# Kernel tuning notes

Hardware: AMD Instinct MI355X
Metric: run time of the kernel (lower is better)

The kernel has to match this reference:

```python
import jax, jax.numpy as jnp
import numpy as np

D_MODEL = 1024
NUM_HEADS = 16
MAX_SEQ_LEN = 2048
THETA = 10000.0
HEAD_DIM = D_MODEL // NUM_HEADS  # 64


def _trunc_normal(key, shape, std):
    # truncated normal in [-3, 3] sigma, matching nn.init.trunc_normal_
    return std * jax.random.truncated_normal(key, -3.0, 3.0, shape, dtype=jnp.float32)


def setup_inputs() -> dict:
    key = jax.random.key(0)
    kx, kq, kk, kv, ko = jax.random.split(key, 5)
    B, L = 2, 2048
    sigma = np.sqrt(2.0 / (D_MODEL + D_MODEL))
    x = jax.random.normal(kx, (B, L, D_MODEL), dtype=jnp.float32)
    token_positions = jnp.arange(L, dtype=jnp.int64 if jax.config.jax_enable_x64 else jnp.int32)[None, :]
    return {
        "x": x,
        "wq": _trunc_normal(kq, (D_MODEL, D_MODEL), sigma),
        "wk": _trunc_normal(kk, (D_MODEL, D_MODEL), sigma),
        "wv": _trunc_normal(kv, (D_MODEL, D_MODEL), sigma),
        "wo": _trunc_normal(ko, (D_MODEL, D_MODEL), sigma),
        "token_positions": token_positions,
    }


def _rope_tables():
    pos = jnp.arange(MAX_SEQ_LEN, dtype=jnp.float32)
    d_idx = jnp.arange(HEAD_DIM // 2, dtype=jnp.float32)
    inv_freq = THETA ** (-2.0 * d_idx / HEAD_DIM)
    angles = pos[:, None] * inv_freq[None, :]  # [max_seq_len, head_dim/2]
    return jnp.cos(angles), jnp.sin(angles)


def _apply_rope(x, cos, sin):
    # x: [b, n, l, h]; cos/sin: [1, l, h/2] (broadcast over b, n)
    xe = x[..., 0::2]
    xo = x[..., 1::2]
    oe = cos * xe - sin * xo
    oo = sin * xe + cos * xo
    # interleave back: stack last axis then flatten pairs
    out = jnp.stack([oe, oo], axis=-1)
    return out.reshape(x.shape)


def reference(x, wq, wk, wv, wo, token_positions):
    B, L, _ = x.shape
    cos_t, sin_t = _rope_tables()
    cos = cos_t[token_positions]  # [1, L, h/2]
    sin = sin_t[token_positions]

    def proj(w):
        y = jnp.einsum('bld,ed->ble', x, w)
        return y.reshape(B, L, NUM_HEADS, HEAD_DIM).transpose(0, 2, 1, 3)  # b n l h

    q, k, v = proj(wq), proj(wk), proj(wv)
    q = _apply_rope(q, cos, sin)
    k = _apply_rope(k, cos, sin)

    scale = 1.0 / np.sqrt(HEAD_DIM).astype(np.float32)
    logits = jnp.einsum('bnqh,bnkh->bnqk', q, k) * scale
    causal = jnp.tril(jnp.ones((L, L), dtype=bool))
    logits = jnp.where(causal[None, None], logits, -jnp.inf)
    scores = jax.nn.softmax(logits, axis=-1)
    out = jnp.einsum('bnqk,bnkh->bnqh', scores, v)
    out = out.transpose(0, 2, 1, 3).reshape(B, L, D_MODEL)
    return jnp.einsum('bld,ed->ble', out, wo)
```

## Files before the change

### kernel.cpp

```cpp
#include <hip/hip_runtime.h>
#include <stdint.h>
#include <stddef.h>

#define SEQ   2048
#define HD    64
#define DM    1024
#define NHEAD 16

typedef __bf16 bf16x8 __attribute__((ext_vector_type(8)));
typedef __bf16 bf16x4 __attribute__((ext_vector_type(4)));
typedef float  f32x4  __attribute__((ext_vector_type(4)));

#define MFMA16x16(a, b, c) __builtin_amdgcn_mfma_f32_16x16x32_bf16((a), (b), (c), 0, 0, 0)

__device__ __forceinline__ void gload16(const void* g, void* lds_uniform) {
    __builtin_amdgcn_global_load_lds(
        (const __attribute__((address_space(1))) uint32_t*)g,
        (__attribute__((address_space(3))) uint32_t*)lds_uniform, 16, 0, 0);
}

__global__ void prep_kernel(const float* __restrict__ x,
                            const float* __restrict__ wq, const float* __restrict__ wk,
                            const float* __restrict__ wv, const float* __restrict__ wo,
                            __bf16* __restrict__ xb, __bf16* __restrict__ wqkv,
                            __bf16* __restrict__ wob, float2* __restrict__ ctst) {
    int bid = blockIdx.x;
    if (bid < 4096) {
        int i = (bid * 256 + threadIdx.x) * 4;
        const float4 v = *(const float4*)(x + i);
        __bf16 o[4] = {(__bf16)v.x, (__bf16)v.y, (__bf16)v.z, (__bf16)v.w};
        *(uint64_t*)(xb + i) = *(const uint64_t*)o;
    } else if (bid < 8192) {
        int g = (bid - 4096) >> 10;
        int i = (((bid - 4096) & 1023) * 256 + threadIdx.x) * 4;
        const float* src = (g == 0) ? wq : (g == 1) ? wk : (g == 2) ? wv : wo;
        __bf16* dst = (g == 3) ? wob : (wqkv + (size_t)g * 1048576);
        const float4 v = *(const float4*)(src + i);
        __bf16 o[4] = {(__bf16)v.x, (__bf16)v.y, (__bf16)v.z, (__bf16)v.w};
        *(uint64_t*)(dst + i) = *(const uint64_t*)o;
    } else {
        int i = (bid - 8192) * 256 + threadIdx.x;
        int p = i & 31;
        int pos = i >> 5;
        float freq = expf(-(float)p * (logf(10000.0f) / 32.0f));
        float ang = (float)pos * freq;
        ctst[i] = make_float2(cosf(ang), sinf(ang));
    }
}

template <int MODE, int BN>
__global__ __launch_bounds__(256, 4)
void gemm_bt_kernel(const __bf16* __restrict__ A, const __bf16* __restrict__ W,
                    float* __restrict__ C, __bf16* __restrict__ Qb,
                    __bf16* __restrict__ Kb, __bf16* __restrict__ VTb,
                    const int* __restrict__ tpos, const float2* __restrict__ ctst,
                    int N, int K) {
    constexpr int NJ = BN >> 5;
    __shared__ __align__(16) char smem[16384 + BN * 128];
    char* As = smem;
    char* Bs = smem + 16384;
    const int lane = threadIdx.x & 63;
    const int w    = threadIdx.x >> 6;

    const int nbn = N / BN;
    const int per = (nbn * 32) >> 3;
    const int id  = blockIdx.x;
    const int lin = (id & 7) * per + (id >> 3);
    const int bm  = lin / nbn;
    const int bn  = lin % nbn;

    const int rbase = (w >> 1) * 64;
    const int cbase = (w & 1) * (BN / 2);

    f32x4 acc[4][NJ] = {};

    const int kt_iters = K >> 6;
    for (int kt = 0; kt < kt_iters; ++kt) {
        #pragma unroll
        for (int c = 0; c < 4; ++c) {
            int id2 = (c * 4 + w) * 64 + lane;
            int row = id2 >> 3, cc = id2 & 7;
            int koff = kt * 64 + ((cc ^ (row & 7)) << 3);
            gload16(A + (size_t)(bm * 128 + row) * K + koff, As + (c * 4 + w) * 1024);
        }
        #pragma unroll
        for (int c = 0; c < NJ; ++c) {
            int id2 = (c * 4 + w) * 64 + lane;
            int row = id2 >> 3, cc = id2 & 7;
            int koff = kt * 64 + ((cc ^ (row & 7)) << 3);
            gload16(W + (size_t)(bn * BN + row) * K + koff, Bs + (c * 4 + w) * 1024);
        }
        __syncthreads();
        #pragma unroll
        for (int ks = 0; ks < 2; ++ks) {
            bf16x8 af[4], bfr[NJ];
            #pragma unroll
            for (int i = 0; i < 4; ++i) {
                int row = rbase + i * 16 + (lane & 15);
                int c = ks * 4 + (lane >> 4);
                af[i] = *(const bf16x8*)(As + row * 128 + ((c ^ (row & 7)) << 4));
            }
            #pragma unroll
            for (int j = 0; j < NJ; ++j) {
                int row = cbase + j * 16 + (lane & 15);
                int c = ks * 4 + (lane >> 4);
                bfr[j] = *(const bf16x8*)(Bs + row * 128 + ((c ^ (row & 7)) << 4));
            }
            #pragma unroll
            for (int i = 0; i < 4; ++i)
                #pragma unroll
                for (int j = 0; j < NJ; ++j)
                    acc[i][j] = MFMA16x16(af[i], bfr[j], acc[i][j]);
        }
        __syncthreads();
    }

    if (MODE == 1) {
        #pragma unroll
        for (int i = 0; i < 4; ++i)
            #pragma unroll
            for (int j = 0; j < NJ; ++j)
                #pragma unroll
                for (int r = 0; r < 4; ++r) {
                    int m = bm * 128 + rbase + i * 16 + (lane >> 4) * 4 + r;
                    int n = bn * BN + cbase + j * 16 + (lane & 15);
                    C[(size_t)m * N + n] = acc[i][j][r];
                }
    } else {
        const int which = bn >> 3;
        char* T = smem + w * 8192;
        #pragma unroll
        for (int i = 0; i < 4; ++i)
            #pragma unroll
            for (int j = 0; j < NJ; ++j)
                #pragma unroll
                for (int r = 0; r < 4; ++r) {
                    int mi = i * 16 + (lane >> 4) * 4 + r;
                    int ni = j * 16 + (lane & 15);
                    __bf16 v = (__bf16)acc[i][j][r];
                    if (which == 2)
                        *(__bf16*)(T + ni * 128 + ((mi * 2) ^ ((ni & 7) << 4))) = v;
                    else
                        *(__bf16*)(T + mi * 128 + ((ni * 2) ^ ((mi & 7) << 4))) = v;
                }
        #pragma unroll
        for (int it = 0; it < 8; ++it) {
            int id2 = it * 64 + lane;
            int row = id2 >> 3, cc = id2 & 7;
            bf16x8 v = *(const bf16x8*)(T + row * 128 + ((cc ^ (row & 7)) << 4));
            if (which == 2) {
                int n = bn * BN + cbase + row;
                int m = bm * 128 + rbase + cc * 8;
                int b = m >> 11, l = m & (SEQ - 1);
                int h = (n & (DM - 1)) >> 6, d = n & 63;
                *(bf16x8*)(VTb + ((size_t)((b * NHEAD + h) * HD + d) * SEQ) + l) = v;
            } else {
                int m = bm * 128 + rbase + row;
                int n = bn * BN + cbase + cc * 8;
                int b = m >> 11, l = m & (SEQ - 1);
                int h = (n & (DM - 1)) >> 6, d = n & 63;
                int pb = tpos[l] * 32 + (d >> 1);
                float sc = (which == 0) ? 0.18033688011112042f : 1.0f;
                bf16x8 ov;
                #pragma unroll
                for (int jj = 0; jj < 4; ++jj) {
                    float2 cs = ctst[pb + jj];
                    float e = (float)v[2 * jj], dd = (float)v[2 * jj + 1];
                    ov[2 * jj]     = (__bf16)(sc * (cs.x * e - cs.y * dd));
                    ov[2 * jj + 1] = (__bf16)(sc * (cs.y * e + cs.x * dd));
                }
                __bf16* dst = which ? Kb : Qb;
                *(bf16x8*)(dst + ((size_t)(b * NHEAD + h) * SEQ + l) * HD + d) = ov;
            }
        }
    }
}

__global__ __launch_bounds__(256, 4)
void attn_kernel(const __bf16* __restrict__ Q, const __bf16* __restrict__ K,
                 const __bf16* __restrict__ VT, __bf16* __restrict__ O) {
    __shared__ __align__(16) char smem[40960];
    const int lane = threadIdx.x & 63;
    const int w    = threadIdx.x >> 6;
    const int tid  = threadIdx.x;
    const int hi   = lane >> 4;
    const int lo   = lane & 15;
    char* Ps = smem + 32768 + w * 2048;

    const int bid = blockIdx.x;
    const int xcd = bid & 7;
    const int idx = bid >> 3;
    const int s   = idx & 31;
    const int r   = idx >> 5;
    const int bh  = xcd * 4 + r;
    const int qb  = (r & 1) ? s : (31 - s);

    const __bf16* Qbh  = Q  + (size_t)bh * SEQ * HD;
    const __bf16* Kbh  = K  + (size_t)bh * SEQ * HD;
    const __bf16* VTbh = VT + (size_t)bh * HD * SEQ;
    const int b = bh >> 4, h = bh & 15;

    #pragma unroll
    for (int c = 0; c < 2; ++c) {
        int id = (c * 4 + w) * 64 + lane;
        int row = id >> 3, cc = id & 7;
        int sw = (cc ^ (row & 7)) << 3;
        gload16(Kbh + (size_t)row * HD + sw, smem + (c * 4 + w) * 1024);
        gload16(VTbh + (size_t)row * SEQ + sw, smem + 8192 + (c * 4 + w) * 1024);
    }

    const int qrow = qb * 64 + w * 16 + lo;
    bf16x8 qf[2];
    qf[0] = *(const bf16x8*)(Qbh + (size_t)qrow * HD + hi * 8);
    qf[1] = *(const bf16x8*)(Qbh + (size_t)qrow * HD + 32 + hi * 8);

    bf16x8 ones;
    #pragma unroll
    for (int i = 0; i < 8; ++i) ones[i] = (__bf16)1.0f;

    f32x4 o[4] = {};
    f32x4 ls = {};
    float mrow = -1e30f;

    int cur = 0;
    __syncthreads();

    for (int kb = 0; kb <= qb; ++kb) {
        bf16x8 kreg[2], vreg[2];
        if (kb < qb) {
            #pragma unroll
            for (int c = 0; c < 2; ++c) {
                int id = c * 256 + tid;
                int row = id >> 3, cc = id & 7;
                kreg[c] = *(const bf16x8*)(Kbh + (size_t)((kb + 1) * 64 + row) * HD + cc * 8);
                vreg[c] = *(const bf16x8*)(VTbh + (size_t)row * SEQ + (kb + 1) * 64 + cc * 8);
            }
        }

        char* Ks = smem + cur * 16384;
        char* Vs = Ks + 8192;

        f32x4 s4[4];
        __builtin_amdgcn_s_setprio(1);
        #pragma unroll
        for (int jt = 0; jt < 4; ++jt) {
            f32x4 z = {};
            #pragma unroll
            for (int ks = 0; ks < 2; ++ks) {
                int row = jt * 16 + lo;
                int c = ks * 4 + hi;
                bf16x8 kf = *(const bf16x8*)(Ks + row * 128 + ((c ^ (row & 7)) << 4));
                z = MFMA16x16(kf, qf[ks], z);
            }
            s4[jt] = z;
        }
        __builtin_amdgcn_s_setprio(0);

        if (kb == qb) {
            int i = qb * 64 + w * 16 + lo;
            #pragma unroll
            for (int jt = 0; jt < 4; ++jt)
                #pragma unroll
                for (int rr = 0; rr < 4; ++rr) {
                    int j = kb * 64 + jt * 16 + hi * 4 + rr;
                    if (j > i) s4[jt][rr] = -1e30f;
                }
        }

        float t0 = fmaxf(fmaxf(fmaxf(s4[0][0], s4[0][1]), s4[0][2]), s4[0][3]);
        float t1 = fmaxf(fmaxf(fmaxf(s4[1][0], s4[1][1]), s4[1][2]), s4[1][3]);
        float t2 = fmaxf(fmaxf(fmaxf(s4[2][0], s4[2][1]), s4[2][2]), s4[2][3]);
        float t3 = fmaxf(fmaxf(fmaxf(s4[3][0], s4[3][1]), s4[3][2]), s4[3][3]);
        float pmax = fmaxf(fmaxf(fmaxf(t0, t1), t2), t3);

        if (!__all(pmax <= mrow + 8.0f)) {
            pmax = fmaxf(pmax, __shfl_xor(pmax, 16));
            pmax = fmaxf(pmax, __shfl_xor(pmax, 32));
            float mn = fmaxf(mrow, pmax);
            float alpha = exp2f(mrow - mn);
            mrow = mn;
            float ar[4];
            #pragma unroll
            for (int rr = 0; rr < 4; ++rr) ar[rr] = __shfl(alpha, hi * 4 + rr);
            #pragma unroll
            for (int rr = 0; rr < 4; ++rr) ls[rr] *= ar[rr];
            #pragma unroll
            for (int dt = 0; dt < 4; ++dt)
                #pragma unroll
                for (int rr = 0; rr < 4; ++rr)
                    o[dt][rr] *= ar[rr];
        }

        {
            int swr = (lo & 7) << 4;
            #pragma unroll
            for (int jt = 0; jt < 4; ++jt) {
                bf16x4 pk;
                #pragma unroll
                for (int rr = 0; rr < 4; ++rr)
                    pk[rr] = (__bf16)exp2f(s4[jt][rr] - mrow);
                int jj = (jt * 16 + hi * 4) * 2;
                *(bf16x4*)(Ps + lo * 128 + (jj ^ swr)) = pk;
            }
        }

        __builtin_amdgcn_s_setprio(1);
        #pragma unroll
        for (int js = 0; js < 2; ++js) {
            int cb = js * 4 + hi;
            bf16x8 pf = *(const bf16x8*)(Ps + lo * 128 + ((cb ^ (lo & 7)) << 4));
            ls = MFMA16x16(pf, ones, ls);
            #pragma unroll
            for (int dt = 0; dt < 4; ++dt) {
                int vrow = dt * 16 + lo;
                bf16x8 vf = *(const bf16x8*)(Vs + vrow * 128 + ((cb ^ (vrow & 7)) << 4));
                o[dt] = MFMA16x16(pf, vf, o[dt]);
            }
        }
        __builtin_amdgcn_s_setprio(0);

        if (kb < qb) {
            char* Kn = smem + (cur ^ 1) * 16384;
            char* Vn = Kn + 8192;
            #pragma unroll
            for (int c = 0; c < 2; ++c) {
                int id = c * 256 + tid;
                int row = id >> 3, cc = id & 7;
                int sw = (cc ^ (row & 7)) << 4;
                *(bf16x8*)(Kn + row * 128 + sw) = kreg[c];
                *(bf16x8*)(Vn + row * 128 + sw) = vreg[c];
            }
        }

        __syncthreads();
        cur ^= 1;
    }

    float linv[4];
    #pragma unroll
    for (int rr = 0; rr < 4; ++rr) linv[rr] = 1.0f / ls[rr];

    char* Os = smem + 32768;
    #pragma unroll
    for (int dt = 0; dt < 4; ++dt)
        #pragma unroll
        for (int rr = 0; rr < 4; ++rr) {
            int orow = w * 16 + hi * 4 + rr;
            int oc = (dt * 16 + lo) * 2;
            *(__bf16*)(Os + orow * 128 + (oc ^ ((orow & 7) << 4))) = (__bf16)(o[dt][rr] * linv[rr]);
        }
    __syncthreads();

    #pragma unroll
    for (int c = 0; c < 2; ++c) {
        int id = c * 256 + tid;
        int row = id >> 3, cc = id & 7;
        bf16x8 v = *(const bf16x8*)(Os + row * 128 + ((cc ^ (row & 7)) << 4));
        *(bf16x8*)(O + (size_t)(b * SEQ + qb * 64 + row) * DM + h * HD + cc * 8) = v;
    }
}

extern "C" void kernel_launch(void* const* d_in, const int* in_sizes, int n_in,
                              void* d_out, int out_size, void* d_ws, size_t ws_size,
                              hipStream_t stream) {
    const float* x  = (const float*)d_in[0];
    const float* wq = (const float*)d_in[1];
    const float* wk = (const float*)d_in[2];
    const float* wv = (const float*)d_in[3];
    const float* wo = (const float*)d_in[4];
    const int* tpos = (const int*)d_in[5];
    float* out = (float*)d_out;
    char* ws = (char*)d_ws;

    __bf16* xb   = (__bf16*)(ws);
    __bf16* wqkv = (__bf16*)(ws + (size_t)(8  << 20));
    __bf16* wob  = (__bf16*)(ws + (size_t)(14 << 20));
    __bf16* Qb   = (__bf16*)(ws + (size_t)(16 << 20));
    __bf16* Kb   = (__bf16*)(ws + (size_t)(24 << 20));
    __bf16* VTb  = (__bf16*)(ws + (size_t)(32 << 20));
    __bf16* Ob   = (__bf16*)(ws + (size_t)(40 << 20));
    float2* ctst = (float2*)(ws + (size_t)(48 << 20));

    prep_kernel<<<8448, 256, 0, stream>>>(x, wq, wk, wv, wo, xb, wqkv, wob, ctst);
    gemm_bt_kernel<0, 128><<<768, 256, 0, stream>>>(xb, wqkv, nullptr, Qb, Kb, VTb,
                                                    tpos, ctst, 3072, 1024);
    attn_kernel<<<1024, 256, 0, stream>>>(Qb, Kb, VTb, Ob);
    gemm_bt_kernel<1, 64><<<512, 256, 0, stream>>>(Ob, wob, out, nullptr, nullptr, nullptr,
                                                   nullptr, nullptr, 1024, 1024);
}
```

Measured before the change: 103.2 us.

## Keep softmax probabilities in registers by permuting V columns in LDS

Removes the per-wave LDS round-trip for the P matrix. The exponentiated scores are packed straight from the QK^T accumulator layout into MFMA A-operands. To make the k-index ordering match, V^T columns are loaded in a permuted order (two 8-byte pieces per 16-byte LDS chunk), and the first V tile is now loaded through registers instead of global_load_lds. LDS usage drops to 32KB, which could allow higher occupancy, but the V loads become narrower 8-byte global accesses.

```diff
diff --git a/kernel.cpp b/kernel.cpp
--- a/kernel.cpp
+++ b/kernel.cpp
@@ -10,6 +10,8 @@
 typedef __bf16 bf16x8 __attribute__((ext_vector_type(8)));
 typedef __bf16 bf16x4 __attribute__((ext_vector_type(4)));
 typedef float  f32x4  __attribute__((ext_vector_type(4)));
+typedef uint32_t u32x2 __attribute__((ext_vector_type(2)));
+typedef uint32_t u32x4 __attribute__((ext_vector_type(4)));
 
 #define MFMA16x16(a, b, c) __builtin_amdgcn_mfma_f32_16x16x32_bf16((a), (b), (c), 0, 0, 0)
 
@@ -179,13 +181,12 @@
 __global__ __launch_bounds__(256, 4)
 void attn_kernel(const __bf16* __restrict__ Q, const __bf16* __restrict__ K,
                  const __bf16* __restrict__ VT, __bf16* __restrict__ O) {
-    __shared__ __align__(16) char smem[40960];
+    __shared__ __align__(16) char smem[32768];
     const int lane = threadIdx.x & 63;
     const int w    = threadIdx.x >> 6;
     const int tid  = threadIdx.x;
     const int hi   = lane >> 4;
     const int lo   = lane & 15;
-    char* Ps = smem + 32768 + w * 2048;
 
     const int bid = blockIdx.x;
     const int xcd = bid & 7;
@@ -200,13 +201,24 @@
     const __bf16* VTbh = VT + (size_t)bh * HD * SEQ;
     const int b = bh >> 4, h = bh & 15;
 
-    #pragma unroll
-    for (int c = 0; c < 2; ++c) {
-        int id = (c * 4 + w) * 64 + lane;
-        int row = id >> 3, cc = id & 7;
-        int sw = (cc ^ (row & 7)) << 3;
-        gload16(Kbh + (size_t)row * HD + sw, smem + (c * 4 + w) * 1024);
-        gload16(VTbh + (size_t)row * SEQ + sw, smem + 8192 + (c * 4 + w) * 1024);
+    {
+        #pragma unroll
+        for (int c = 0; c < 2; ++c) {
+            int id = c * 256 + tid;
+            int row = id >> 3, cc = id & 7;
+            int sw = (cc ^ (row & 7)) << 3;
+            gload16(Kbh + (size_t)row * HD + sw, smem + (c * 4 + w) * 1024);
+        }
+        #pragma unroll
+        for (int c = 0; c < 2; ++c) {
+            int id = c * 256 + tid;
+            int row = id >> 3, cc = id & 7;
+            int jA = ((cc >> 2) << 5) | ((cc & 3) << 2);
+            u32x2 a = *(const u32x2*)(VTbh + (size_t)row * SEQ + jA);
+            u32x2 bq = *(const u32x2*)(VTbh + (size_t)row * SEQ + jA + 16);
+            u32x4 v4 = {a[0], a[1], bq[0], bq[1]};
+            *(u32x4*)(smem + 8192 + row * 128 + ((cc ^ (row & 7)) << 4)) = v4;
+        }
     }
 
     const int qrow = qb * 64 + w * 16 + lo;
@@ -226,14 +238,19 @@
     __syncthreads();
 
     for (int kb = 0; kb <= qb; ++kb) {
-        bf16x8 kreg[2], vreg[2];
+        bf16x8 kreg[2];
+        u32x4  vreg[2];
         if (kb < qb) {
             #pragma unroll
             for (int c = 0; c < 2; ++c) {
                 int id = c * 256 + tid;
                 int row = id >> 3, cc = id & 7;
                 kreg[c] = *(const bf16x8*)(Kbh + (size_t)((kb + 1) * 64 + row) * HD + cc * 8);
-                vreg[c] = *(const bf16x8*)(VTbh + (size_t)row * SEQ + (kb + 1) * 64 + cc * 8);
+                int jA = ((cc >> 2) << 5) | ((cc & 3) << 2);
+                const __bf16* vsrc = VTbh + (size_t)row * SEQ + (kb + 1) * 64 + jA;
+                u32x2 a = *(const u32x2*)(vsrc);
+                u32x2 bq = *(const u32x2*)(vsrc + 16);
+                vreg[c] = u32x4{a[0], a[1], bq[0], bq[1]};
             }
         }
 
@@ -291,30 +308,23 @@
                     o[dt][rr] *= ar[rr];
         }
 
-        {
-            int swr = (lo & 7) << 4;
-            #pragma unroll
-            for (int jt = 0; jt < 4; ++jt) {
-                bf16x4 pk;
-                #pragma unroll
-                for (int rr = 0; rr < 4; ++rr)
-                    pk[rr] = (__bf16)exp2f(s4[jt][rr] - mrow);
-                int jj = (jt * 16 + hi * 4) * 2;
-                *(bf16x4*)(Ps + lo * 128 + (jj ^ swr)) = pk;
-            }
-        }
+        bf16x8 pk8[2];
+        #pragma unroll
+        for (int js = 0; js < 2; ++js)
+            #pragma unroll
+            for (int e = 0; e < 8; ++e)
+                pk8[js][e] = (__bf16)exp2f(s4[2 * js + (e >> 2)][e & 3] - mrow);
 
         __builtin_amdgcn_s_setprio(1);
         #pragma unroll
         for (int js = 0; js < 2; ++js) {
+            ls = MFMA16x16(pk8[js], ones, ls);
             int cb = js * 4 + hi;
-            bf16x8 pf = *(const bf16x8*)(Ps + lo * 128 + ((cb ^ (lo & 7)) << 4));
-            ls = MFMA16x16(pf, ones, ls);
             #pragma unroll
             for (int dt = 0; dt < 4; ++dt) {
                 int vrow = dt * 16 + lo;
                 bf16x8 vf = *(const bf16x8*)(Vs + vrow * 128 + ((cb ^ (vrow & 7)) << 4));
-                o[dt] = MFMA16x16(pf, vf, o[dt]);
+                o[dt] = MFMA16x16(pk8[js], vf, o[dt]);
             }
         }
         __builtin_amdgcn_s_setprio(0);
@@ -328,7 +338,7 @@
                 int row = id >> 3, cc = id & 7;
                 int sw = (cc ^ (row & 7)) << 4;
                 *(bf16x8*)(Kn + row * 128 + sw) = kreg[c];
-                *(bf16x8*)(Vn + row * 128 + sw) = vreg[c];
+                *(u32x4*)(Vn + row * 128 + sw) = vreg[c];
             }
         }
 
@@ -340,7 +350,7 @@
     #pragma unroll
     for (int rr = 0; rr < 4; ++rr) linv[rr] = 1.0f / ls[rr];
 
-    char* Os = smem + 32768;
+    char* Os = smem;
     #pragma unroll
     for (int dt = 0; dt < 4; ++dt)
         #pragma unroll
```

Result: no change. 101.5 us (-1.6%).
